# Performance work log

Hardware: AMD Instinct MI355X
Metric: run time of the kernel (lower is better)

The kernel has to match this reference:

```python
import jax, jax.numpy as jnp
import numpy as np

EMBED = 1024
HEADS = 16
HDIM = 64
FF = 4 * EMBED
EPS = 1e-5


def layer_norm(x, g, b):
    mu = jnp.mean(x, axis=-1, keepdims=True)
    var = jnp.var(x, axis=-1, keepdims=True)
    return (x - mu) * jax.lax.rsqrt(var + EPS) * g + b


def setup_inputs() -> dict:
    key = jax.random.key(0)
    ks = jax.random.split(key, 12)
    s = lambda fan_in: 1.0 / np.sqrt(fan_in)
    return {
        "x": jax.random.normal(ks[0], (2, 2048, EMBED), jnp.float32),
        "w_qkv": jax.random.uniform(ks[1], (EMBED, 3 * HEADS * HDIM), jnp.float32, -s(EMBED), s(EMBED)),
        "w_proj": jax.random.uniform(ks[2], (HEADS * HDIM, EMBED), jnp.float32, -s(HEADS * HDIM), s(HEADS * HDIM)),
        "b_proj": jax.random.uniform(ks[3], (EMBED,), jnp.float32, -s(HEADS * HDIM), s(HEADS * HDIM)),
        "w1": jax.random.uniform(ks[4], (EMBED, FF), jnp.float32, -s(EMBED), s(EMBED)),
        "b1": jax.random.uniform(ks[5], (FF,), jnp.float32, -s(EMBED), s(EMBED)),
        "w2": jax.random.uniform(ks[6], (FF, EMBED), jnp.float32, -s(FF), s(FF)),
        "b2": jax.random.uniform(ks[7], (EMBED,), jnp.float32, -s(FF), s(FF)),
        "g1": jnp.ones((EMBED,), jnp.float32),
        "be1": jnp.zeros((EMBED,), jnp.float32),
        "g2": jnp.ones((EMBED,), jnp.float32),
        "be2": jnp.zeros((EMBED,), jnp.float32),
    }


def reference(x, w_qkv, w_proj, b_proj, w1, b1, w2, b2, g1, be1, g2, be2):
    bs, seq, _ = x.shape
    # --- MHA on pre-norm ---
    h = layer_norm(x, g1, be1)
    qkv = h @ w_qkv  # [b, s, 3*H*D]
    qkv = qkv.reshape(bs, seq, HEADS, 3, HDIM)
    q = qkv[:, :, :, 0, :]  # [b, s, h, d]
    k = qkv[:, :, :, 1, :]
    v = qkv[:, :, :, 2, :]
    attn = jnp.einsum("bqhd,bkhd->bhqk", q, k) / np.sqrt(HDIM)
    causal = jnp.tril(jnp.ones((seq, seq), bool))
    attn = jnp.where(causal, attn, -jnp.inf)
    attn = jax.nn.softmax(attn, axis=-1)
    out = jnp.einsum("bhqk,bkhd->bhqd", attn, v)
    # Faithful to original bug: .view without transposing heads back.
    out = out.reshape(bs, seq, HEADS * HDIM)
    out = out @ w_proj + b_proj
    x = x + out
    # --- FFN on pre-norm ---
    h2 = layer_norm(x, g2, be2)
    ff = jax.nn.relu(h2 @ w1 + b1) @ w2 + b2
    return x + ff
```

## Files before the change

kernel.cpp:

```cpp
#include <hip/hip_runtime.h>
#include <cstdint>

#define EMBED 1024
#define HEADS 16
#define HDIM  64
#define SEQ   2048
#define BATCH 2
#define ROWS  (BATCH*SEQ)

typedef __bf16 bf16x8 __attribute__((ext_vector_type(8)));
typedef float  f32x4  __attribute__((ext_vector_type(4)));
typedef float  f32x16 __attribute__((ext_vector_type(16)));
typedef unsigned int uint32x2 __attribute__((ext_vector_type(2)));

__device__ __forceinline__ unsigned short f2bf(float f) {
    union { float f; uint32_t u; } v; v.f = f;
    uint32_t r = v.u + 0x7fffu + ((v.u >> 16) & 1u);
    return (unsigned short)(r >> 16);
}

__device__ __forceinline__ uint32_t cvtpk_bf16(float lo, float hi) {
    uint32_t r;
    asm("v_cvt_pk_bf16_f32 %0, %1, %2" : "=v"(r) : "v"(lo), "v"(hi));
    return r;
}

__device__ __forceinline__ float fexp2(float x) {
    float r;
    asm("v_exp_f32 %0, %1" : "=v"(r) : "v"(x));
    return r;
}

#define GLDS(src, dst) __builtin_amdgcn_global_load_lds( \
    (const __attribute__((address_space(1))) uint32_t*)(src), \
    (__attribute__((address_space(3))) uint32_t*)(dst), 16, 0, 0)

__global__ __launch_bounds__(256) void k_transpose_all(
    const float* __restrict__ w_qkv, const float* __restrict__ w_proj,
    const float* __restrict__ w1,    const float* __restrict__ w2,
    unsigned short* __restrict__ wqkvT, unsigned short* __restrict__ wprojT,
    unsigned short* __restrict__ w1T,   unsigned short* __restrict__ w2T)
{
    int b = blockIdx.x;
    const float* in; unsigned short* out; int N, K, nx;
    if (b < 3072)      {           in = w_qkv;  out = wqkvT;  K = 1024; N = 3072; nx = 96; }
    else if (b < 4096) { b -= 3072; in = w_proj; out = wprojT; K = 1024; N = 1024; nx = 32; }
    else if (b < 8192) { b -= 4096; in = w1;     out = w1T;    K = 1024; N = 4096; nx = 128; }
    else               { b -= 8192; in = w2;     out = w2T;    K = 4096; N = 1024; nx = 32; }
    const int n0 = (b % nx) * 32, k0 = (b / nx) * 32;

    __shared__ float tile[32][33];
    const int tx = threadIdx.x & 31, ty = threadIdx.x >> 5;
#pragma unroll
    for (int r = 0; r < 4; ++r)
        tile[ty + 8*r][tx] = in[(size_t)(k0 + ty + 8*r) * N + n0 + tx];
    __syncthreads();
#pragma unroll
    for (int r = 0; r < 4; ++r)
        out[(size_t)(n0 + ty + 8*r) * K + k0 + tx] = f2bf(tile[tx][ty + 8*r]);
}

__global__ __launch_bounds__(256) void k_layernorm(
    const float* __restrict__ x, const float* __restrict__ g, const float* __restrict__ b,
    unsigned short* __restrict__ h)
{
    const int row = blockIdx.x, t = threadIdx.x;
    float4 v = ((const float4*)(x + (size_t)row * EMBED))[t];
    float s = v.x + v.y + v.z + v.w;
    float q = v.x*v.x + v.y*v.y + v.z*v.z + v.w*v.w;
#pragma unroll
    for (int off = 32; off >= 1; off >>= 1) {
        s += __shfl_xor(s, off, 64);
        q += __shfl_xor(q, off, 64);
    }
    __shared__ float ss[4], sq[4];
    if ((t & 63) == 0) { ss[t >> 6] = s; sq[t >> 6] = q; }
    __syncthreads();
    s = ss[0] + ss[1] + ss[2] + ss[3];
    q = sq[0] + sq[1] + sq[2] + sq[3];
    const float mu  = s * (1.0f / EMBED);
    const float var = q * (1.0f / EMBED) - mu * mu;
    const float rs  = rsqrtf(var + 1e-5f);
    float4 gv = ((const float4*)g)[t];
    float4 bv = ((const float4*)b)[t];
    ushort4 o;
    o.x = f2bf((v.x - mu) * rs * gv.x + bv.x);
    o.y = f2bf((v.y - mu) * rs * gv.y + bv.y);
    o.z = f2bf((v.z - mu) * rs * gv.z + bv.z);
    o.w = f2bf((v.w - mu) * rs * gv.w + bv.w);
    ((ushort4*)(h + (size_t)row * EMBED))[t] = o;
}

template<int FLAGS, typename OutT>
__global__ __launch_bounds__(512) void k_gemm_bt(
    const unsigned short* __restrict__ A,
    const unsigned short* __restrict__ BT,
    const float* __restrict__ bias,
    const float* __restrict__ resid,
    OutT* __restrict__ C,
    int M, int N, int K)
{
    __shared__ uint4 ldsv[8192];
    char* base = (char*)ldsv;
    char* aL = base;
    char* bL = base + 16384;
    const int t = threadIdx.x, l = t & 63, w = t >> 6;
    const int pos = w & 3, kh = w >> 2;
    const int qr = pos >> 1, qc = pos & 1;
    const int g = l >> 4, c = l & 15;

    const int gx = gridDim.x;
    const int lin = blockIdx.y * gx + blockIdx.x;
    const int cpx = (gx * gridDim.y) >> 3;
    const int swz = (lin & 7) * cpx + (lin >> 3);
    const int row0 = (swz / gx) * 128, col0 = (swz % gx) * 128;

    const int swc = (((l & 7) ^ (l >> 3)) * 8);
    const int rA0 = w*16 + (l >> 3), rA1 = rA0 + 8;
    const unsigned short* aS0 = A  + (size_t)(row0 + rA0) * K + swc;
    const unsigned short* aS1 = A  + (size_t)(row0 + rA1) * K + swc;
    const unsigned short* bS0 = BT + (size_t)(col0 + rA0) * K + swc;
    const unsigned short* bS1 = BT + (size_t)(col0 + rA1) * K + swc;
    const int dst0 = w * 2048, dst1 = w * 2048 + 1024;

    f32x4 acc[4][4];
#pragma unroll
    for (int m = 0; m < 4; ++m)
#pragma unroll
        for (int n = 0; n < 4; ++n) acc[m][n] = f32x4{0.f, 0.f, 0.f, 0.f};

    auto stage = [&](int kt, int bo) {
        const size_t ko = (size_t)kt * 64;
        GLDS(aS0 + ko, aL + bo + dst0);
        GLDS(aS1 + ko, aL + bo + dst1);
        GLDS(bS0 + ko, bL + bo + dst0);
        GLDS(bS1 + ko, bL + bo + dst1);
    };
    auto compute = [&](int bo) {
        const int chb = ((kh*4 + g) ^ (c & 7)) * 16;
        bf16x8 af[4], bfr[4];
#pragma unroll
        for (int m = 0; m < 4; ++m)
            af[m] = *(const bf16x8*)(aL + bo + (qr*64 + m*16 + c) * 128 + chb);
#pragma unroll
        for (int n = 0; n < 4; ++n)
            bfr[n] = *(const bf16x8*)(bL + bo + (qc*64 + n*16 + c) * 128 + chb);
        __builtin_amdgcn_s_setprio(1);
#pragma unroll
        for (int m = 0; m < 4; ++m)
#pragma unroll
            for (int n = 0; n < 4; ++n)
                acc[m][n] = __builtin_amdgcn_mfma_f32_16x16x32_bf16(af[m], bfr[n], acc[m][n], 0, 0, 0);
        __builtin_amdgcn_s_setprio(0);
    };

    const int nkt = K >> 6;
    stage(0, 0);
    stage(1, 32768);
    for (int kt = 0; kt < nkt; ++kt) {
        const int bo = (kt & 3) * 32768;
        if (kt + 2 < nkt) {
            stage(kt + 2, ((kt + 2) & 3) * 32768);
            asm volatile("s_waitcnt vmcnt(8)" ::: "memory");
        } else if (kt + 1 < nkt) {
            asm volatile("s_waitcnt vmcnt(4)" ::: "memory");
        } else {
            asm volatile("s_waitcnt vmcnt(0)" ::: "memory");
        }
        __builtin_amdgcn_s_barrier();
        compute(bo);
    }

    asm volatile("s_waitcnt lgkmcnt(0)" ::: "memory");
    __builtin_amdgcn_s_barrier();
    if (kh) {
#pragma unroll
        for (int m = 0; m < 4; ++m)
#pragma unroll
            for (int n = 0; n < 4; ++n)
                *(f32x4*)(base + (((pos*16 + m*4 + n) * 64) + l) * 16) = acc[m][n];
    }
    asm volatile("s_waitcnt lgkmcnt(0)" ::: "memory");
    __builtin_amdgcn_s_barrier();

    if (!kh) {
#pragma unroll
        for (int m = 0; m < 4; ++m) {
            const int rb = row0 + qr*64 + m*16 + g*4;
#pragma unroll
            for (int n = 0; n < 4; ++n) {
                const f32x4 part = *(const f32x4*)(base + (((pos*16 + m*4 + n) * 64) + l) * 16);
                const int col = col0 + qc*64 + n*16 + c;
                float bv = 0.f;
                if constexpr ((FLAGS & 1) != 0) bv = bias[col];
#pragma unroll
                for (int j = 0; j < 4; ++j) {
                    float v = acc[m][n][j] + part[j] + bv;
                    if constexpr ((FLAGS & 2) != 0) v = fmaxf(v, 0.f);
                    if constexpr ((FLAGS & 4) != 0) v += resid[(size_t)(rb + j) * N + col];
                    if constexpr (sizeof(OutT) == 2) C[(size_t)(rb + j) * N + col] = (OutT)f2bf(v);
                    else                             C[(size_t)(rb + j) * N + col] = v;
                }
            }
        }
    }
}

template<int FLAGS, typename OutT>
__global__ __launch_bounds__(512) __attribute__((amdgpu_waves_per_eu(2, 2)))
void k_gemm256(
    const unsigned short* __restrict__ A,
    const unsigned short* __restrict__ BT,
    const float* __restrict__ bias,
    OutT* __restrict__ C,
    unsigned short* __restrict__ Qo,
    unsigned short* __restrict__ Ko,
    unsigned short* __restrict__ Vo,
    int M, int N, int K)
{
    __shared__ uint4 ldsv[8192];
    char* base = (char*)ldsv;
    const int t = threadIdx.x, l = t & 63, w = t >> 6;
    const int wr = w >> 2, wc = w & 3;
    const int g = l >> 4, c = l & 15;

    const int gx = gridDim.x;
    const int lin = blockIdx.y * gx + blockIdx.x;
    const int cpx = (gx * gridDim.y) >> 3;
    const int swz = (lin & 7) * cpx + (lin >> 3);
    const int row0 = (swz / gx) * 256, col0 = (swz % gx) * 256;

    const int sr = l >> 3, sc = l & 7;
    const int swk = (sc ^ sr) * 8;
    const unsigned short* aSr = A  + (size_t)(row0 + w*32 + sr) * K + swk;
    const unsigned short* bSr = BT + (size_t)(col0 + w*32 + sr) * K + swk;

    f32x4 acc[8][4];
#pragma unroll
    for (int m = 0; m < 8; ++m)
#pragma unroll
        for (int n = 0; n < 4; ++n) acc[m][n] = f32x4{0.f, 0.f, 0.f, 0.f};

    auto stage = [&](int kt, int bo) {
        const size_t ko = (size_t)kt * 64;
#pragma unroll
        for (int i = 0; i < 4; ++i) {
            GLDS(aSr + ko + (size_t)(i*8) * K, base + bo + (w*4 + i)*1024);
            GLDS(bSr + ko + (size_t)(i*8) * K, base + bo + 32768 + (w*4 + i)*1024);
        }
    };

    const int nkt = K >> 6;
    stage(0, 0);
    asm volatile("s_waitcnt vmcnt(0)" ::: "memory");
    __builtin_amdgcn_s_barrier();
    int bufo = 0;
    for (int kt = 0; kt < nkt; ++kt) {
        if (kt + 1 < nkt) stage(kt + 1, bufo ^ 65536);
        bf16x8 bfr[4][2];
#pragma unroll
        for (int n = 0; n < 4; ++n)
#pragma unroll
            for (int ks = 0; ks < 2; ++ks) {
                const int r = wc*64 + n*16 + c;
                bfr[n][ks] = *(const bf16x8*)(base + bufo + 32768 + r*128
                                              + (((ks*4 + g) ^ (c & 7)) * 16));
            }
#pragma unroll
        for (int p = 0; p < 4; ++p) {
            bf16x8 af[2][2];
#pragma unroll
            for (int mi = 0; mi < 2; ++mi)
#pragma unroll
                for (int ks = 0; ks < 2; ++ks) {
                    const int r = wr*128 + (p*2 + mi)*16 + c;
                    af[mi][ks] = *(const bf16x8*)(base + bufo + r*128
                                                  + (((ks*4 + g) ^ (c & 7)) * 16));
                }
            __builtin_amdgcn_s_setprio(1);
#pragma unroll
            for (int ks = 0; ks < 2; ++ks)
#pragma unroll
                for (int mi = 0; mi < 2; ++mi)
#pragma unroll
                    for (int n = 0; n < 4; ++n)
                        acc[p*2 + mi][n] = __builtin_amdgcn_mfma_f32_16x16x32_bf16(
                            af[mi][ks], bfr[n][ks], acc[p*2 + mi][n], 0, 0, 0);
            __builtin_amdgcn_s_setprio(0);
        }
        if (kt + 1 < nkt) {
            asm volatile("s_waitcnt vmcnt(0)" ::: "memory");
            __builtin_amdgcn_s_barrier();
            bufo ^= 65536;
        }
    }

    if constexpr ((FLAGS & 8) != 0) {
#pragma unroll
        for (int m = 0; m < 8; ++m) {
            const int rb = row0 + wr*128 + m*16 + g*4;
            const int b  = rb >> 11;
            const int q0 = rb & 2047;
#pragma unroll
            for (int n = 0; n < 4; ++n) {
                const int col = col0 + wc*64 + n*16 + c;
                const int hh  = col / 192;
                const int rem = col - hh * 192;
                const int tt  = rem >> 6;
                const int d   = rem & 63;
                const int bhh = b * HEADS + hh;
                if (tt == 2) {
                    const int st_e = q0 >> 6, kk = q0 & 63;
                    const int f_e  = (d >> 5) * 4 + (kk >> 4);
                    const int ln_e = ((kk >> 3) & 1) * 32 + (d & 31);
                    const int e0   = kk & 7;
                    ushort4 o;
                    o.x = f2bf(acc[m][n][0]); o.y = f2bf(acc[m][n][1]);
                    o.z = f2bf(acc[m][n][2]); o.w = f2bf(acc[m][n][3]);
                    *(ushort4*)(Vo + (size_t)bhh * (SEQ*HDIM) + st_e*4096 + f_e*512 + ln_e*8 + e0) = o;
                } else if (tt == 1) {
                    const int st_e = q0 >> 6;
                    const int f_e  = ((q0 >> 5) & 1) * 4 + (d >> 4);
                    const int lq_e = q0 & 31;
                    const int ln_b = ((d >> 3) & 1) * 32;
                    const int e_e  = d & 7;
                    unsigned short* dst = Ko + (size_t)bhh * (SEQ*HDIM) + st_e*4096 + f_e*512
                                             + (ln_b + lq_e)*8 + e_e;
#pragma unroll
                    for (int j = 0; j < 4; ++j)
                        dst[j*8] = f2bf(acc[m][n][j]);
                } else {
                    unsigned short* dst = Qo + ((size_t)bhh * SEQ + q0) * HDIM + d;
#pragma unroll
                    for (int j = 0; j < 4; ++j)
                        dst[(size_t)j * HDIM] = f2bf(acc[m][n][j]);
                }
            }
        }
    } else {
#pragma unroll
        for (int m = 0; m < 8; ++m) {
            const int rb = row0 + wr*128 + m*16 + g*4;
#pragma unroll
            for (int n = 0; n < 4; ++n) {
                const int col = col0 + wc*64 + n*16 + c;
                float bv = 0.f;
                if constexpr ((FLAGS & 1) != 0) bv = bias[col];
#pragma unroll
                for (int j = 0; j < 4; ++j) {
                    float v = acc[m][n][j] + bv;
                    if constexpr ((FLAGS & 2) != 0) v = fmaxf(v, 0.f);
                    if constexpr (sizeof(OutT) == 2) C[(size_t)(rb + j) * N + col] = (OutT)f2bf(v);
                    else                             C[(size_t)(rb + j) * N + col] = v;
                }
            }
        }
    }
}

__global__ __launch_bounds__(512) __attribute__((amdgpu_waves_per_eu(2, 2)))
void k_attention(
    const unsigned short* __restrict__ Qb,
    const unsigned short* __restrict__ Kf,
    const unsigned short* __restrict__ Vf,
    unsigned short* __restrict__ out)
{
    const int t = threadIdx.x, l = t & 63, w = t >> 6;
    const int lq = l & 31, hi = l >> 5;
    const int bid = blockIdx.x;
    const int sbid = (bid & 7) * 32 + (bid >> 3);
    const int bh = sbid >> 3, j = sbid & 7;
    const int qb = (w < 4) ? (4*j + w) : (63 - 4*j - (w - 4));
    const int q  = qb * 32 + lq;

    const unsigned short* Qh  = Qb + (size_t)bh * SEQ * HDIM;
    const unsigned short* Kfh = Kf + (size_t)bh * SEQ * HDIM + l*8;
    const unsigned short* Vfh = Vf + (size_t)bh * SEQ * HDIM + l*8;

    const bf16x8 qf0 = *(const bf16x8*)(Qh + (size_t)q * HDIM      + hi*8);
    const bf16x8 qf1 = *(const bf16x8*)(Qh + (size_t)q * HDIM + 16 + hi*8);
    const bf16x8 qf2 = *(const bf16x8*)(Qh + (size_t)q * HDIM + 32 + hi*8);
    const bf16x8 qf3 = *(const bf16x8*)(Qh + (size_t)q * HDIM + 48 + hi*8);

    f32x16 oT0, oT1;
#pragma unroll
    for (int i = 0; i < 16; ++i) { oT0[i] = 0.f; oT1[i] = 0.f; }
    float lacc0 = 0.f, lacc1 = 0.f, lacc2 = 0.f, lacc3 = 0.f;
    const float kSc = 0.18033688011112042f;
    const int nst = (qb >> 1) + 1;

    bf16x8 kA0, kA1, kA2, kA3, kA4, kA5, kA6, kA7;
    bf16x8 kB0, kB1, kB2, kB3, kB4, kB5, kB6, kB7;

#define LOADK(stv, KF) do {                                                     \
    const unsigned short* kp_ = Kfh + (size_t)(stv) * 4096;                     \
    KF##0 = *(const bf16x8*)(kp_ +    0); KF##1 = *(const bf16x8*)(kp_ +  512); \
    KF##2 = *(const bf16x8*)(kp_ + 1024); KF##3 = *(const bf16x8*)(kp_ + 1536); \
    KF##4 = *(const bf16x8*)(kp_ + 2048); KF##5 = *(const bf16x8*)(kp_ + 2560); \
    KF##6 = *(const bf16x8*)(kp_ + 3072); KF##7 = *(const bf16x8*)(kp_ + 3584); \
} while (0)

#define STEP(stv, KF) do {                                                      \
    const int kv0_ = (stv) * 64;                                                \
    const unsigned short* vp_ = Vfh + (size_t)(stv) * 4096;                     \
    bf16x8 vf0_ = *(const bf16x8*)(vp_ +    0), vf1_ = *(const bf16x8*)(vp_ +  512); \
    bf16x8 vf2_ = *(const bf16x8*)(vp_ + 1024), vf3_ = *(const bf16x8*)(vp_ + 1536); \
    bf16x8 vf4_ = *(const bf16x8*)(vp_ + 2048), vf5_ = *(const bf16x8*)(vp_ + 2560); \
    bf16x8 vf6_ = *(const bf16x8*)(vp_ + 3072), vf7_ = *(const bf16x8*)(vp_ + 3584); \
    f32x16 sA_, sB_;                                                            \
    _Pragma("unroll")                                                           \
    for (int i = 0; i < 16; ++i) { sA_[i] = 0.f; sB_[i] = 0.f; }               \
    __builtin_amdgcn_s_setprio(1);                                              \
    sA_ = __builtin_amdgcn_mfma_f32_32x32x16_bf16(KF##0, qf0, sA_, 0, 0, 0);    \
    sA_ = __builtin_amdgcn_mfma_f32_32x32x16_bf16(KF##1, qf1, sA_, 0, 0, 0);    \
    sA_ = __builtin_amdgcn_mfma_f32_32x32x16_bf16(KF##2, qf2, sA_, 0, 0, 0);    \
    sA_ = __builtin_amdgcn_mfma_f32_32x32x16_bf16(KF##3, qf3, sA_, 0, 0, 0);    \
    sB_ = __builtin_amdgcn_mfma_f32_32x32x16_bf16(KF##4, qf0, sB_, 0, 0, 0);    \
    sB_ = __builtin_amdgcn_mfma_f32_32x32x16_bf16(KF##5, qf1, sB_, 0, 0, 0);    \
    sB_ = __builtin_amdgcn_mfma_f32_32x32x16_bf16(KF##6, qf2, sB_, 0, 0, 0);    \
    sB_ = __builtin_amdgcn_mfma_f32_32x32x16_bf16(KF##7, qf3, sB_, 0, 0, 0);    \
    __builtin_amdgcn_s_setprio(0);                                              \
    float p_[32];                                                               \
    if ((stv) == nst - 1) {                                                     \
        _Pragma("unroll")                                                       \
        for (int r = 0; r < 16; ++r) {                                          \
            const int key_ = kv0_ + (r & 3) + 8*(r >> 2) + 4*hi;                \
            p_[r]      = (key_      <= q) ? fexp2(sA_[r] * kSc) : 0.f;          \
            p_[16 + r] = (key_ + 32 <= q) ? fexp2(sB_[r] * kSc) : 0.f;          \
        }                                                                       \
    } else {                                                                    \
        _Pragma("unroll")                                                       \
        for (int r = 0; r < 16; ++r) {                                          \
            p_[r]      = fexp2(sA_[r] * kSc);                                   \
            p_[16 + r] = fexp2(sB_[r] * kSc);                                   \
        }                                                                       \
    }                                                                           \
    _Pragma("unroll")                                                           \
    for (int i = 0; i < 32; i += 4) {                                           \
        lacc0 += p_[i]; lacc1 += p_[i+1]; lacc2 += p_[i+2]; lacc3 += p_[i+3];   \
    }                                                                           \
    bf16x8 pa_[4];                                                              \
    _Pragma("unroll")                                                           \
    for (int ks = 0; ks < 4; ++ks) {                                            \
        const int b8_ = ks * 8;                                                 \
        uint32x2 rA_ = __builtin_amdgcn_permlane32_swap(                        \
            cvtpk_bf16(p_[b8_+0], p_[b8_+1]), cvtpk_bf16(p_[b8_+4], p_[b8_+5]), false, false); \
        uint32x2 rB_ = __builtin_amdgcn_permlane32_swap(                        \
            cvtpk_bf16(p_[b8_+2], p_[b8_+3]), cvtpk_bf16(p_[b8_+6], p_[b8_+7]), false, false); \
        union { uint32_t u[4]; bf16x8 v; } pk_;                                 \
        pk_.u[0] = rA_[0]; pk_.u[1] = rB_[0]; pk_.u[2] = rA_[1]; pk_.u[3] = rB_[1]; \
        pa_[ks] = pk_.v;                                                        \
    }                                                                           \
    __builtin_amdgcn_s_setprio(1);                                              \
    oT0 = __builtin_amdgcn_mfma_f32_32x32x16_bf16(vf0_, pa_[0], oT0, 0, 0, 0);  \
    oT0 = __builtin_amdgcn_mfma_f32_32x32x16_bf16(vf1_, pa_[1], oT0, 0, 0, 0);  \
    oT0 = __builtin_amdgcn_mfma_f32_32x32x16_bf16(vf2_, pa_[2], oT0, 0, 0, 0);  \
    oT0 = __builtin_amdgcn_mfma_f32_32x32x16_bf16(vf3_, pa_[3], oT0, 0, 0, 0);  \
    oT1 = __builtin_amdgcn_mfma_f32_32x32x16_bf16(vf4_, pa_[0], oT1, 0, 0, 0);  \
    oT1 = __builtin_amdgcn_mfma_f32_32x32x16_bf16(vf5_, pa_[1], oT1, 0, 0, 0);  \
    oT1 = __builtin_amdgcn_mfma_f32_32x32x16_bf16(vf6_, pa_[2], oT1, 0, 0, 0);  \
    oT1 = __builtin_amdgcn_mfma_f32_32x32x16_bf16(vf7_, pa_[3], oT1, 0, 0, 0);  \
    __builtin_amdgcn_s_setprio(0);                                              \
} while (0)

    LOADK(0, kA);
    int st = 0;
    for (;;) {
        if (st + 1 < nst) LOADK(st + 1, kB);
        STEP(st, kA);
        if (++st >= nst) break;
        if (st + 1 < nst) LOADK(st + 1, kA);
        STEP(st, kB);
        if (++st >= nst) break;
    }
#undef LOADK
#undef STEP

    float lsum = (lacc0 + lacc1) + (lacc2 + lacc3);
    lsum += __shfl_xor(lsum, 32, 64);
    const float inv = 1.f / lsum;
    unsigned short* ob = out + ((size_t)bh * SEQ + q) * HDIM;
#pragma unroll
    for (int m2 = 0; m2 < 4; ++m2) {
        ushort4 o0, o1;
        o0.x = f2bf(oT0[m2*4+0] * inv); o0.y = f2bf(oT0[m2*4+1] * inv);
        o0.z = f2bf(oT0[m2*4+2] * inv); o0.w = f2bf(oT0[m2*4+3] * inv);
        o1.x = f2bf(oT1[m2*4+0] * inv); o1.y = f2bf(oT1[m2*4+1] * inv);
        o1.z = f2bf(oT1[m2*4+2] * inv); o1.w = f2bf(oT1[m2*4+3] * inv);
        *(ushort4*)(ob +      m2*8 + hi*4) = o0;
        *(ushort4*)(ob + 32 + m2*8 + hi*4) = o1;
    }
}

extern "C" void kernel_launch(void* const* d_in, const int* in_sizes, int n_in,
                              void* d_out, int out_size, void* d_ws, size_t ws_size,
                              hipStream_t stream)
{
    (void)in_sizes; (void)n_in; (void)out_size; (void)ws_size;
    const float* x      = (const float*)d_in[0];
    const float* w_qkv  = (const float*)d_in[1];
    const float* w_proj = (const float*)d_in[2];
    const float* b_proj = (const float*)d_in[3];
    const float* w1     = (const float*)d_in[4];
    const float* b1     = (const float*)d_in[5];
    const float* w2     = (const float*)d_in[6];
    const float* b2     = (const float*)d_in[7];
    const float* g1     = (const float*)d_in[8];
    const float* be1    = (const float*)d_in[9];
    const float* g2     = (const float*)d_in[10];
    const float* be2    = (const float*)d_in[11];

    char* ws = (char*)d_ws;
    size_t o = 0;
    auto take = [&](size_t bytes) -> char* {
        char* p = ws + o;
        o += (bytes + 255) & ~(size_t)255;
        return p;
    };
    unsigned short* wqkvT  = (unsigned short*)take(3072ull * 1024 * 2);
    unsigned short* wprojT = (unsigned short*)take(1024ull * 1024 * 2);
    unsigned short* w1T    = (unsigned short*)take(4096ull * 1024 * 2);
    unsigned short* w2T    = (unsigned short*)take(1024ull * 4096 * 2);
    unsigned short* h      = (unsigned short*)take(4096ull * 1024 * 2);
    unsigned short* Qb     = (unsigned short*)take(4096ull * 1024 * 2);
    unsigned short* Kfb    = (unsigned short*)take(4096ull * 1024 * 2);
    unsigned short* Vfb    = (unsigned short*)take(4096ull * 1024 * 2);
    unsigned short* attno  = (unsigned short*)take(4096ull * 1024 * 2);
    float*          x2     = (float*)take(4096ull * 1024 * 4);
    unsigned short* f1     = Qb;

    k_transpose_all<<<12288, 256, 0, stream>>>(
        w_qkv, w_proj, w1, w2, wqkvT, wprojT, w1T, w2T);

    k_layernorm<<<4096, 256, 0, stream>>>(x, g1, be1, h);
    k_gemm256<8, unsigned short><<<dim3(12, 16), 512, 0, stream>>>(
        h, wqkvT, nullptr, (unsigned short*)nullptr, Qb, Kfb, Vfb, ROWS, 3072, 1024);
    k_attention<<<256, 512, 0, stream>>>(Qb, Kfb, Vfb, attno);
    k_gemm_bt<5, float><<<dim3(8, 32), 512, 0, stream>>>(
        attno, wprojT, b_proj, x, x2, ROWS, 1024, 1024);
    k_layernorm<<<4096, 256, 0, stream>>>(x2, g2, be2, h);
    k_gemm256<3, unsigned short><<<dim3(16, 16), 512, 0, stream>>>(
        h, w1T, b1, f1, nullptr, nullptr, nullptr, ROWS, 4096, 1024);
    k_gemm_bt<5, float><<<dim3(8, 32), 512, 0, stream>>>(
        f1, w2T, b2, x2, (float*)d_out, ROWS, 1024, 4096);
}
```

Measured before the change: 181.3 us.

## Switch GEMM mainloop to 4-buffer K=32 pipeline with two stages in flight

The GEMM main loop now stages K-slices of 32 instead of 64 into four rotating LDS buffers, keeping two stages of global-to-LDS loads in flight with partial vmcnt waits instead of a full drain every iteration. The LDS layout and XOR swizzle change to 64-byte rows, and each wave loads all A/B fragments at once per slice. The aim is to hide global load latency behind MFMA work. The cost is twice as many barriers per K, and with only one barrier per iteration the buffer being overwritten depends on the 4-deep ring leaving enough slack.

```diff
diff --git a/kernel.cpp b/kernel.cpp
--- a/kernel.cpp
+++ b/kernel.cpp
@@ -230,10 +230,13 @@
     const int swz = (lin & 7) * cpx + (lin >> 3);
     const int row0 = (swz / gx) * 256, col0 = (swz % gx) * 256;
 
-    const int sr = l >> 3, sc = l & 7;
-    const int swk = (sc ^ sr) * 8;
-    const unsigned short* aSr = A  + (size_t)(row0 + w*32 + sr) * K + swk;
-    const unsigned short* bSr = BT + (size_t)(col0 + w*32 + sr) * K + swk;
+    const int srow = l >> 2;
+    const int sch  = (l & 3) ^ ((l >> 3) & 3);
+    const unsigned short* aS0 = A  + (size_t)(row0 + w*32 +      srow) * K + sch*8;
+    const unsigned short* aS1 = A  + (size_t)(row0 + w*32 + 16 + srow) * K + sch*8;
+    const unsigned short* bS0 = BT + (size_t)(col0 + w*32 +      srow) * K + sch*8;
+    const unsigned short* bS1 = BT + (size_t)(col0 + w*32 + 16 + srow) * K + sch*8;
+    const int dA0 = w*2048, dA1 = w*2048 + 1024;
 
     f32x4 acc[8][4];
 #pragma unroll
@@ -242,57 +245,45 @@
         for (int n = 0; n < 4; ++n) acc[m][n] = f32x4{0.f, 0.f, 0.f, 0.f};
 
     auto stage = [&](int kt, int bo) {
-        const size_t ko = (size_t)kt * 64;
-#pragma unroll
-        for (int i = 0; i < 4; ++i) {
-            GLDS(aSr + ko + (size_t)(i*8) * K, base + bo + (w*4 + i)*1024);
-            GLDS(bSr + ko + (size_t)(i*8) * K, base + bo + 32768 + (w*4 + i)*1024);
+        const size_t ko = (size_t)kt * 32;
+        GLDS(aS0 + ko, base + bo + dA0);
+        GLDS(aS1 + ko, base + bo + dA1);
+        GLDS(bS0 + ko, base + bo + 16384 + dA0);
+        GLDS(bS1 + ko, base + bo + 16384 + dA1);
+    };
+    auto compute = [&](int bo) {
+        const int chb = (g ^ ((c >> 1) & 3)) * 16;
+        bf16x8 af[8], bfr[4];
+#pragma unroll
+        for (int m = 0; m < 8; ++m)
+            af[m] = *(const bf16x8*)(base + bo + (wr*128 + m*16 + c) * 64 + chb);
+#pragma unroll
+        for (int n = 0; n < 4; ++n)
+            bfr[n] = *(const bf16x8*)(base + bo + 16384 + (wc*64 + n*16 + c) * 64 + chb);
+        __builtin_amdgcn_s_setprio(1);
+#pragma unroll
+        for (int m = 0; m < 8; ++m)
+#pragma unroll
+            for (int n = 0; n < 4; ++n)
+                acc[m][n] = __builtin_amdgcn_mfma_f32_16x16x32_bf16(af[m], bfr[n], acc[m][n], 0, 0, 0);
+        __builtin_amdgcn_s_setprio(0);
+    };
+
+    const int nkt = K >> 5;
+    stage(0, 0);
+    stage(1, 32768);
+    for (int kt = 0; kt < nkt; ++kt) {
+        const int bo = (kt & 3) * 32768;
+        if (kt + 2 < nkt) {
+            stage(kt + 2, ((kt + 2) & 3) * 32768);
+            asm volatile("s_waitcnt vmcnt(8)" ::: "memory");
+        } else if (kt + 1 < nkt) {
+            asm volatile("s_waitcnt vmcnt(4)" ::: "memory");
+        } else {
+            asm volatile("s_waitcnt vmcnt(0)" ::: "memory");
         }
-    };
-
-    const int nkt = K >> 6;
-    stage(0, 0);
-    asm volatile("s_waitcnt vmcnt(0)" ::: "memory");
-    __builtin_amdgcn_s_barrier();
-    int bufo = 0;
-    for (int kt = 0; kt < nkt; ++kt) {
-        if (kt + 1 < nkt) stage(kt + 1, bufo ^ 65536);
-        bf16x8 bfr[4][2];
-#pragma unroll
-        for (int n = 0; n < 4; ++n)
-#pragma unroll
-            for (int ks = 0; ks < 2; ++ks) {
-                const int r = wc*64 + n*16 + c;
-                bfr[n][ks] = *(const bf16x8*)(base + bufo + 32768 + r*128
-                                              + (((ks*4 + g) ^ (c & 7)) * 16));
-            }
-#pragma unroll
-        for (int p = 0; p < 4; ++p) {
-            bf16x8 af[2][2];
-#pragma unroll
-            for (int mi = 0; mi < 2; ++mi)
-#pragma unroll
-                for (int ks = 0; ks < 2; ++ks) {
-                    const int r = wr*128 + (p*2 + mi)*16 + c;
-                    af[mi][ks] = *(const bf16x8*)(base + bufo + r*128
-                                                  + (((ks*4 + g) ^ (c & 7)) * 16));
-                }
-            __builtin_amdgcn_s_setprio(1);
-#pragma unroll
-            for (int ks = 0; ks < 2; ++ks)
-#pragma unroll
-                for (int mi = 0; mi < 2; ++mi)
-#pragma unroll
-                    for (int n = 0; n < 4; ++n)
-                        acc[p*2 + mi][n] = __builtin_amdgcn_mfma_f32_16x16x32_bf16(
-                            af[mi][ks], bfr[n][ks], acc[p*2 + mi][n], 0, 0, 0);
-            __builtin_amdgcn_s_setprio(0);
-        }
-        if (kt + 1 < nkt) {
-            asm volatile("s_waitcnt vmcnt(0)" ::: "memory");
-            __builtin_amdgcn_s_barrier();
-            bufo ^= 65536;
-        }
+        __builtin_amdgcn_s_barrier();
+        compute(bo);
     }
 
     if constexpr ((FLAGS & 8) != 0) {
```

After: 181.4 us. Within noise of the previous version (+0.1%).
